# Performance work log

Hardware: AMD Instinct MI355X
Metric: run time of the kernel (lower is better)

The kernel has to match this reference:

```python
import jax, jax.numpy as jnp
import numpy as np

EPS = 1e-5  # BatchNorm1d default eps
NUM_HEADS = 8


def repbn(x, alpha, gamma, beta, rm, rv):
    # eval-mode RepBN over the channel (last) dim: BN(running stats) + alpha * x
    bn = (x - rm) * (gamma / jnp.sqrt(rv + EPS)) + beta
    return bn + alpha * x


def _forward(x, W_qkv, b_qkv, W_proj, b_proj, W1, b1, W2, b2, sa_w, sa_b,
             alpha1, gamma1, beta1, rm1, rv1, alpha2, gamma2, beta2, rm2, rv2):
    B, C, H, W = x.shape
    N = H * W
    D = C // NUM_HEADS
    t = x.reshape(B, C, N).transpose(0, 2, 1)  # [B, N, C]
    # --- FlashAttention (manual MHSA) ---
    qkv = (t @ W_qkv + b_qkv).reshape(B, N, 3, NUM_HEADS, D)
    q = qkv[:, :, 0].transpose(0, 2, 1, 3)  # [B, h, N, D]
    k = qkv[:, :, 1].transpose(0, 2, 1, 3)
    v = qkv[:, :, 2].transpose(0, 2, 1, 3)
    attn = jax.nn.softmax(jnp.einsum('bhnd,bhmd->bhnm', q, k) * (D ** -0.5), axis=-1)
    o = jnp.einsum('bhnm,bhmd->bhnd', attn, v).transpose(0, 2, 1, 3).reshape(B, N, C)
    o = o @ W_proj + b_proj
    # residual + blended norm (eval -> RepBN)
    t = repbn(t + o, alpha1, gamma1, beta1, rm1, rv1)
    # --- FFN with SpatialSILU activation ---
    h = t @ W1 + b1  # [B, N, cm]
    # depthwise 1x1 conv over the batch dim (channels==B per original unsqueeze(0))
    wgt = sa_w[:, None, None] * h + sa_b[:, None, None]
    h = h * jax.nn.sigmoid(wgt * h)
    f = h @ W2 + b2
    t = repbn(t + f, alpha2, gamma2, beta2, rm2, rv2)
    return t.transpose(0, 2, 1).reshape(B, C, H, W)


def setup_inputs() -> dict:
    key = jax.random.key(0)
    ks = jax.random.split(key, 8)
    B, C, H, W = 256, 256, 14, 14
    cm = 2048
    s = 0.02
    f32 = jnp.float32
    return {
        'x': jax.random.normal(ks[0], (B, C, H, W), f32),
        'W_qkv': jax.random.normal(ks[1], (C, 3 * C), f32) * s,
        'b_qkv': jnp.zeros((3 * C,), f32),
        'W_proj': jax.random.normal(ks[2], (C, C), f32) * s,
        'b_proj': jnp.zeros((C,), f32),
        'W1': jax.random.normal(ks[3], (C, cm), f32) * s,
        'b1': jnp.zeros((cm,), f32),
        'W2': jax.random.normal(ks[4], (cm, C), f32) * s,
        'b2': jnp.zeros((C,), f32),
        'sa_w': jax.random.normal(ks[5], (B,), f32) * s,
        'sa_b': jnp.zeros((B,), f32),
        'alpha1': jnp.ones((), f32),
        'gamma1': jnp.ones((C,), f32),
        'beta1': jnp.zeros((C,), f32),
        'rm1': jax.random.normal(ks[6], (C,), f32) * 0.1,
        'rv1': jnp.ones((C,), f32),
        'alpha2': jnp.ones((), f32),
        'gamma2': jnp.ones((C,), f32),
        'beta2': jnp.zeros((C,), f32),
        'rm2': jax.random.normal(ks[7], (C,), f32) * 0.1,
        'rv2': jnp.ones((C,), f32),
    }


def reference(x, W_qkv, b_qkv, W_proj, b_proj, W1, b1, W2, b2, sa_w, sa_b,
              alpha1, gamma1, beta1, rm1, rv1, alpha2, gamma2, beta2, rm2, rv2):
    return _forward(x, W_qkv, b_qkv, W_proj, b_proj, W1, b1, W2, b2, sa_w, sa_b,
                    alpha1, gamma1, beta1, rm1, rv1, alpha2, gamma2, beta2, rm2, rv2)
```

## Files before the change

kernel.cpp:

```cpp
#include <hip/hip_runtime.h>

using u16 = unsigned short;

typedef __bf16 bf16x8 __attribute__((ext_vector_type(8)));
typedef u16    u16x8  __attribute__((ext_vector_type(8)));
typedef float  f32x4  __attribute__((ext_vector_type(4)));

__device__ __forceinline__ float b2f(u16 u) {
    union { unsigned int i; float f; } c; c.i = ((unsigned int)u) << 16; return c.f;
}
__device__ __forceinline__ u16 f2b(float f) {
    union { float f; unsigned int i; } c; c.f = f;
    unsigned int i = c.i;
    return (u16)((i + 0x7FFFu + ((i >> 16) & 1u)) >> 16);
}

#define AS1 __attribute__((address_space(1)))
#define AS3 __attribute__((address_space(3)))
__device__ __forceinline__ void glds16(const u16* g, u16* l) {
    __builtin_amdgcn_global_load_lds((const AS1 void*)(const void*)g,
                                     (AS3 void*)(void*)l, 16, 0, 0);
}

__global__ void btrans_f2b(const float* __restrict__ in, u16* __restrict__ out, int R, int C) {
    __shared__ u16 tile[32][33];
    const int c0 = blockIdx.x * 32, r0 = blockIdx.y * 32;
    const size_t base = (size_t)blockIdx.z * R * C;
    const int tx = threadIdx.x, ty = threadIdx.y;
    #pragma unroll
    for (int i = ty; i < 32; i += 8) {
        int r = r0 + i, c = c0 + tx;
        tile[i][tx] = (r < R && c < C) ? f2b(in[base + (size_t)r * C + c]) : (u16)0;
    }
    __syncthreads();
    #pragma unroll
    for (int i = ty; i < 32; i += 8) {
        int c = c0 + i, r = r0 + tx;
        if (c < C && r < R) out[base + (size_t)c * R + r] = tile[tx][i];
    }
}

__global__ void btrans_b2f(const u16* __restrict__ in, float* __restrict__ out, int R, int C) {
    __shared__ u16 tile[32][33];
    const int c0 = blockIdx.x * 32, r0 = blockIdx.y * 32;
    const size_t base = (size_t)blockIdx.z * R * C;
    const int tx = threadIdx.x, ty = threadIdx.y;
    #pragma unroll
    for (int i = ty; i < 32; i += 8) {
        int r = r0 + i, c = c0 + tx;
        tile[i][tx] = (r < R && c < C) ? in[base + (size_t)r * C + c] : (u16)0;
    }
    __syncthreads();
    #pragma unroll
    for (int i = ty; i < 32; i += 8) {
        int c = c0 + i, r = r0 + tx;
        if (c < C && r < R) out[base + (size_t)c * R + r] = b2f(tile[tx][i]);
    }
}

template<int EPI>
__launch_bounds__(512, 4)
__global__ void gemm_bt(const u16* __restrict__ A, const u16* __restrict__ BT,
                        const float* __restrict__ bias, u16* __restrict__ C,
                        int M, int N, int K, int row0,
                        const u16* __restrict__ R0,
                        const float* __restrict__ g, const float* __restrict__ be,
                        const float* __restrict__ rmv, const float* __restrict__ rvv,
                        const float* __restrict__ alpha,
                        const float* __restrict__ saw, const float* __restrict__ sab) {
    __shared__ __align__(16) u16 ALds[2][128 * 32];
    __shared__ __align__(16) u16 BLds[2][128 * 32];
    const int tid  = threadIdx.x;
    const int wave = tid >> 6, lane = tid & 63;
    const int wm = wave >> 2, wn = wave & 3;
    const int quad = lane >> 4, l16 = lane & 15;

    const unsigned gx = gridDim.x;
    unsigned lin = blockIdx.y * gx + blockIdx.x;
    const unsigned nwg = gx * gridDim.y;
    const unsigned q8 = nwg >> 3, r8 = nwg & 7;
    const unsigned xcd = lin & 7, loc = lin >> 3;
    lin = (xcd < r8 ? xcd * (q8 + 1) : r8 * (q8 + 1) + (xcd - r8) * q8) + loc;
    const int m0 = (int)(lin / gx) * 128, n0 = (int)(lin % gx) * 128;

    const int srow = lane >> 2;
    const int scol = (((lane & 3) ^ ((srow >> 1) & 3)) * 8);
    const size_t aoff = (size_t)(m0 + wave * 16 + srow) * K + scol;
    const size_t boff = (size_t)(n0 + wave * 16 + srow) * K + scol;
    u16* aS = &ALds[0][0] + wave * 512;
    u16* bS = &BLds[0][0] + wave * 512;

    const int cfrag = (quad ^ ((l16 >> 1) & 3)) * 8;

    auto stage = [&](int buf, size_t kn) {
        const int bo = buf * 4096;
        glds16(A  + aoff + kn, aS + bo);
        glds16(BT + boff + kn, bS + bo);
    };

    f32x4 acc[4][2] = {};
    const int niter = K >> 5;

    stage(0, 0);

    for (int kt = 0; kt < niter; kt++) {
        const int cur = kt & 1, nxt = cur ^ 1;
        __syncthreads();
        if (kt + 1 < niter) stage(nxt, (size_t)(kt + 1) << 5);
        bf16x8 af[4], bfr[2];
        const u16* ab = &ALds[0][0] + cur * 4096;
        const u16* bb = &BLds[0][0] + cur * 4096;
        #pragma unroll
        for (int i = 0; i < 4; i++)
            af[i] = *(const bf16x8*)&ab[(wm * 64 + i * 16 + l16) * 32 + cfrag];
        #pragma unroll
        for (int j = 0; j < 2; j++)
            bfr[j] = *(const bf16x8*)&bb[(wn * 32 + j * 16 + l16) * 32 + cfrag];
        #pragma unroll
        for (int i = 0; i < 4; i++)
            #pragma unroll
            for (int j = 0; j < 2; j++)
                acc[i][j] = __builtin_amdgcn_mfma_f32_16x16x32_bf16(af[i], bfr[j], acc[i][j], 0, 0, 0);
    }

    float alphav = 0.f;
    if (EPI == 1) alphav = alpha[0];

    #pragma unroll
    for (int i = 0; i < 4; i++) {
        const int rowb = m0 + wm * 64 + i * 16 + quad * 4;
        #pragma unroll
        for (int r = 0; r < 4; r++) {
            const int row = rowb + r;
            float swv = 0.f, sbv = 0.f;
            if (EPI == 2) { int bidx = (row0 + row) / 196; swv = saw[bidx]; sbv = sab[bidx]; }
            #pragma unroll
            for (int j = 0; j < 2; j++) {
                const int col = n0 + wn * 32 + j * 16 + l16;
                float v = acc[i][j][r] + bias[col];
                const size_t off = (size_t)row * N + col;
                if (EPI == 0) {
                    C[off] = f2b(v);
                } else if (EPI == 1) {
                    float x  = v + b2f(R0[off]);
                    float sc = g[col] * rsqrtf(rvv[col] + 1e-5f);
                    float t  = (x - rmv[col]) * sc + be[col] + alphav * x;
                    C[off]  = f2b(t);
                } else {
                    float w   = swv * v + sbv;
                    float out = v / (1.f + __expf(-w * v));
                    C[off] = f2b(out);
                }
            }
        }
    }
}

__launch_bounds__(256)
__global__ void attn_kernel(const u16* __restrict__ qkv, u16* __restrict__ o) {
    __shared__ __align__(16) u16 Kb[224 * 32];
    __shared__ __align__(16) u16 Vt[32 * 232];
    __shared__ __align__(16) u16 Pl[4][16 * 232];
    const int tid  = threadIdx.x;
    const int wave = tid >> 6, lane = tid & 63;
    const int quad = lane >> 4, l16 = lane & 15;
    const int b = blockIdx.x >> 3, h = blockIdx.x & 7;
    const u16* qg = qkv + (size_t)b * 196 * 768 + h * 32;
    const float scale = 0.17677669529663687f;

    for (int idx = tid; idx < 896; idx += 256) {
        int row = idx >> 2, dp = (idx & 3) * 8;
        u16x8 kv = {};
        if (row < 196) kv = *(const u16x8*)&qg[(size_t)row * 768 + 256 + dp];
        *(u16x8*)&Kb[row * 32 + dp] = kv;
    }
    for (int idx = tid; idx < 224 * 32; idx += 256) {
        int row = idx >> 5, d = idx & 31;
        Vt[d * 232 + row] = (row < 196) ? qg[(size_t)row * 768 + 512 + d] : (u16)0;
    }
    for (int c = lane; c < 16 * 24; c += 64) {
        int m = c / 24, cc = 208 + (c % 24);
        Pl[wave][m * 232 + cc] = 0;
    }
    __syncthreads();

    for (int t = wave; t < 13; t += 4) {
        const int m0 = t * 16;
        bf16x8 aq = {};
        const int qrow = m0 + l16;
        if (qrow < 196) aq = *(const bf16x8*)&qg[(size_t)qrow * 768 + quad * 8];

        f32x4 s[13];
        #pragma unroll
        for (int ct = 0; ct < 13; ct++) {
            bf16x8 bk = *(const bf16x8*)&Kb[(ct * 16 + l16) * 32 + quad * 8];
            s[ct] = __builtin_amdgcn_mfma_f32_16x16x32_bf16(aq, bk, (f32x4){0.f, 0.f, 0.f, 0.f}, 0, 0, 0);
        }
        if (l16 >= 4) {
            #pragma unroll
            for (int r = 0; r < 4; r++) s[12][r] = -1e30f;
        }
        float mx[4] = {-1e30f, -1e30f, -1e30f, -1e30f};
        #pragma unroll
        for (int ct = 0; ct < 13; ct++)
            #pragma unroll
            for (int r = 0; r < 4; r++) mx[r] = fmaxf(mx[r], s[ct][r]);
        #pragma unroll
        for (int off = 1; off < 16; off <<= 1)
            #pragma unroll
            for (int r = 0; r < 4; r++) mx[r] = fmaxf(mx[r], __shfl_xor(mx[r], off, 64));
        float sum[4] = {0.f, 0.f, 0.f, 0.f};
        #pragma unroll
        for (int ct = 0; ct < 13; ct++) {
            #pragma unroll
            for (int r = 0; r < 4; r++) {
                float p = __expf((s[ct][r] - mx[r]) * scale);
                sum[r] += p;
                Pl[wave][(quad * 4 + r) * 232 + ct * 16 + l16] = f2b(p);
            }
        }
        #pragma unroll
        for (int off = 1; off < 16; off <<= 1)
            #pragma unroll
            for (int r = 0; r < 4; r++) sum[r] += __shfl_xor(sum[r], off, 64);
        float inv[4];
        #pragma unroll
        for (int r = 0; r < 4; r++) inv[r] = 1.f / sum[r];

        #pragma unroll
        for (int nt = 0; nt < 2; nt++) {
            f32x4 ao = {0.f, 0.f, 0.f, 0.f};
            #pragma unroll
            for (int kc = 0; kc < 7; kc++) {
                bf16x8 ap = *(const bf16x8*)&Pl[wave][l16 * 232 + kc * 32 + quad * 8];
                bf16x8 bv = *(const bf16x8*)&Vt[(nt * 16 + l16) * 232 + kc * 32 + quad * 8];
                ao = __builtin_amdgcn_mfma_f32_16x16x32_bf16(ap, bv, ao, 0, 0, 0);
            }
            #pragma unroll
            for (int r = 0; r < 4; r++) {
                const int gm = m0 + quad * 4 + r;
                if (gm < 196)
                    o[((size_t)b * 196 + gm) * 256 + h * 32 + nt * 16 + l16] = f2b(ao[r] * inv[r]);
            }
        }
    }
}

extern "C" void kernel_launch(void* const* d_in, const int* in_sizes, int n_in,
                              void* d_out, int out_size, void* d_ws, size_t ws_size,
                              hipStream_t stream) {
    const float* x      = (const float*)d_in[0];
    const float* Wqkv   = (const float*)d_in[1];
    const float* bqkv   = (const float*)d_in[2];
    const float* Wproj  = (const float*)d_in[3];
    const float* bproj  = (const float*)d_in[4];
    const float* W1     = (const float*)d_in[5];
    const float* b1     = (const float*)d_in[6];
    const float* W2     = (const float*)d_in[7];
    const float* b2     = (const float*)d_in[8];
    const float* saw    = (const float*)d_in[9];
    const float* sab    = (const float*)d_in[10];
    const float* alpha1 = (const float*)d_in[11];
    const float* g1     = (const float*)d_in[12];
    const float* be1    = (const float*)d_in[13];
    const float* rm1    = (const float*)d_in[14];
    const float* rv1    = (const float*)d_in[15];
    const float* alpha2 = (const float*)d_in[16];
    const float* g2     = (const float*)d_in[17];
    const float* be2    = (const float*)d_in[18];
    const float* rm2    = (const float*)d_in[19];
    const float* rv2    = (const float*)d_in[20];

    const int B = 256, Cc = 256, Np = 196, CM = 2048;
    const int M = B * Np;

    auto al = [](size_t s) { return (s + 255) & ~(size_t)255; };
    char* ws = (char*)d_ws;
    const size_t o_t0  = 0;
    const size_t o_t1  = o_t0 + al((size_t)M * Cc * 2);
    const size_t o_wq  = o_t1 + al((size_t)M * Cc * 2);
    const size_t o_wp  = o_wq + al((size_t)768 * Cc * 2);
    const size_t o_w1  = o_wp + al((size_t)Cc * Cc * 2);
    const size_t o_w2  = o_w1 + al((size_t)Cc * CM * 2);
    const size_t o_scr = o_w2 + al((size_t)CM * Cc * 2);
    const size_t S = (ws_size > o_scr) ? ws_size - o_scr : 0;

    u16* t0     = (u16*)(ws + o_t0);
    u16* t1b    = (u16*)(ws + o_t1);
    u16* WqkvT  = (u16*)(ws + o_wq);
    u16* WprojT = (u16*)(ws + o_wp);
    u16* W1T    = (u16*)(ws + o_w1);
    u16* W2T    = (u16*)(ws + o_w2);
    u16* scr    = (u16*)(ws + o_scr);
    u16* t2     = t0;
    u16* obuf   = (u16*)d_out;
    float* out  = (float*)d_out;

    int nq = 1; while (nq < 8 && ((size_t)(M / nq) * 768 * 2) > S) nq *= 2;
    const int nf_opts[7] = {1, 2, 4, 8, 14, 28, 56};
    int nf = 56;
    for (int i = 0; i < 7; ++i) {
        if (((size_t)(M / nf_opts[i]) * CM * 2) <= S) { nf = nf_opts[i]; break; }
    }
    const int Mq = M / nq, Bq = B / nq;
    const int Mf = M / nf;

    dim3 tb(32, 8, 1);
    btrans_f2b<<<dim3((Np + 31) / 32, (Cc + 31) / 32, B), tb, 0, stream>>>(x, t0, Cc, Np);
    btrans_f2b<<<dim3(768 / 32, Cc / 32, 1), tb, 0, stream>>>(Wqkv,  WqkvT,  Cc, 768);
    btrans_f2b<<<dim3(Cc  / 32, Cc / 32, 1), tb, 0, stream>>>(Wproj, WprojT, Cc, Cc);
    btrans_f2b<<<dim3(CM  / 32, Cc / 32, 1), tb, 0, stream>>>(W1,    W1T,    Cc, CM);
    btrans_f2b<<<dim3(Cc  / 32, CM / 32, 1), tb, 0, stream>>>(W2,    W2T,    CM, Cc);

    for (int c = 0; c < nq; ++c) {
        gemm_bt<0><<<dim3(768 / 128, Mq / 128), 512, 0, stream>>>(
            t0 + (size_t)c * Mq * Cc, WqkvT, bqkv, scr, Mq, 768, Cc, 0,
            nullptr, nullptr, nullptr, nullptr, nullptr, nullptr, nullptr, nullptr);
        attn_kernel<<<dim3(Bq * 8), 256, 0, stream>>>(scr, obuf + (size_t)c * Mq * Cc);
    }

    gemm_bt<1><<<dim3(Cc / 128, M / 128), 512, 0, stream>>>(
        obuf, WprojT, bproj, t1b, M, Cc, Cc, 0,
        t0, g1, be1, rm1, rv1, alpha1, nullptr, nullptr);

    for (int c = 0; c < nf; ++c) {
        gemm_bt<2><<<dim3(CM / 128, Mf / 128), 512, 0, stream>>>(
            t1b + (size_t)c * Mf * Cc, W1T, b1, scr, Mf, CM, Cc, c * Mf,
            nullptr, nullptr, nullptr, nullptr, nullptr, nullptr, saw, sab);
        gemm_bt<1><<<dim3(Cc / 128, Mf / 128), 512, 0, stream>>>(
            scr, W2T, b2, t2 + (size_t)c * Mf * Cc, Mf, Cc, CM, 0,
            t1b + (size_t)c * Mf * Cc, g2, be2, rm2, rv2, alpha2, nullptr, nullptr);
    }

    btrans_b2f<<<dim3((Cc + 31) / 32, (Np + 31) / 32, B), tb, 0, stream>>>(t2, out, Np, Cc);
}
```

Measured before the change: 572.4 us.

## Restructure GEMM epilogue with packed bf16 stores and LDS-staged residual

New measurement: 542.9 us. 5.2% less time.

```diff
diff --git a/kernel.cpp b/kernel.cpp
--- a/kernel.cpp
+++ b/kernel.cpp
@@ -13,6 +13,9 @@
     union { float f; unsigned int i; } c; c.f = f;
     unsigned int i = c.i;
     return (u16)((i + 0x7FFFu + ((i >> 16) & 1u)) >> 16);
+}
+__device__ __forceinline__ float u2f(unsigned int u) {
+    union { unsigned int i; float f; } c; c.i = u; return c.f;
 }
 
 #define AS1 __attribute__((address_space(1)))
@@ -68,8 +71,7 @@
                         const float* __restrict__ rmv, const float* __restrict__ rvv,
                         const float* __restrict__ alpha,
                         const float* __restrict__ saw, const float* __restrict__ sab) {
-    __shared__ __align__(16) u16 ALds[2][128 * 32];
-    __shared__ __align__(16) u16 BLds[2][128 * 32];
+    __shared__ __align__(16) u16 SL[16384];
     const int tid  = threadIdx.x;
     const int wave = tid >> 6, lane = tid & 63;
     const int wm = wave >> 2, wn = wave & 3;
@@ -87,10 +89,13 @@
     const int scol = (((lane & 3) ^ ((srow >> 1) & 3)) * 8);
     const size_t aoff = (size_t)(m0 + wave * 16 + srow) * K + scol;
     const size_t boff = (size_t)(n0 + wave * 16 + srow) * K + scol;
-    u16* aS = &ALds[0][0] + wave * 512;
-    u16* bS = &BLds[0][0] + wave * 512;
+    u16* aS = SL + wave * 512;
+    u16* bS = SL + 8192 + wave * 512;
 
     const int cfrag = (quad ^ ((l16 >> 1) & 3)) * 8;
+
+    f32x4 acc[4][2] = {};
+    const int niter = K >> 5;
 
     auto stage = [&](int buf, size_t kn) {
         const int bo = buf * 4096;
@@ -98,18 +103,12 @@
         glds16(BT + boff + kn, bS + bo);
     };
 
-    f32x4 acc[4][2] = {};
-    const int niter = K >> 5;
-
-    stage(0, 0);
-
-    for (int kt = 0; kt < niter; kt++) {
-        const int cur = kt & 1, nxt = cur ^ 1;
+    auto kstep = [&](int cur, int kt) {
         __syncthreads();
-        if (kt + 1 < niter) stage(nxt, (size_t)(kt + 1) << 5);
+        if (kt + 1 < niter) stage(cur ^ 1, (size_t)(kt + 1) << 5);
+        const u16* ab = SL + cur * 4096;
+        const u16* bb = SL + 8192 + cur * 4096;
         bf16x8 af[4], bfr[2];
-        const u16* ab = &ALds[0][0] + cur * 4096;
-        const u16* bb = &BLds[0][0] + cur * 4096;
         #pragma unroll
         for (int i = 0; i < 4; i++)
             af[i] = *(const bf16x8*)&ab[(wm * 64 + i * 16 + l16) * 32 + cfrag];
@@ -121,37 +120,83 @@
             #pragma unroll
             for (int j = 0; j < 2; j++)
                 acc[i][j] = __builtin_amdgcn_mfma_f32_16x16x32_bf16(af[i], bfr[j], acc[i][j], 0, 0, 0);
-    }
+    };
+
+    stage(0, 0);
+    int kt = 0;
+    for (; kt + 2 <= niter; kt += 2) { kstep(0, kt); kstep(1, kt + 1); }
+    if (kt < niter) kstep(kt & 1, kt);
+
+    __syncthreads();
 
     float alphav = 0.f;
     if (EPI == 1) alphav = alpha[0];
 
+    if (EPI == 1) {
+        #pragma unroll
+        for (int c = tid; c < 2048; c += 512) {
+            int row = c >> 4, colc = (c & 15) * 8;
+            *(u16x8*)&SL[row * 128 + colc] =
+                *(const u16x8*)&R0[(size_t)(m0 + row) * N + n0 + colc];
+        }
+        __syncthreads();
+    }
+
+    float biasv[2], k0v[2], k1v[2];
+    #pragma unroll
+    for (int j = 0; j < 2; j++) {
+        const int col = n0 + wn * 32 + j * 16 + l16;
+        biasv[j] = bias[col];
+        if (EPI == 1) {
+            float sc = g[col] * rsqrtf(rvv[col] + 1e-5f);
+            k1v[j] = sc + alphav;
+            k0v[j] = be[col] - rmv[col] * sc;
+        }
+    }
+
+    const int dup = l16 & 1;
+    const int pr  = l16 >> 1;
+    u16* Crow = C + (size_t)(m0 + wm * 64 + quad * 4 + 2 * dup) * N
+                  + (n0 + wn * 32 + pr * 2);
+
     #pragma unroll
     for (int i = 0; i < 4; i++) {
-        const int rowb = m0 + wm * 64 + i * 16 + quad * 4;
-        #pragma unroll
-        for (int r = 0; r < 4; r++) {
-            const int row = rowb + r;
-            float swv = 0.f, sbv = 0.f;
-            if (EPI == 2) { int bidx = (row0 + row) / 196; swv = saw[bidx]; sbv = sab[bidx]; }
-            #pragma unroll
-            for (int j = 0; j < 2; j++) {
-                const int col = n0 + wn * 32 + j * 16 + l16;
-                float v = acc[i][j][r] + bias[col];
-                const size_t off = (size_t)row * N + col;
-                if (EPI == 0) {
-                    C[off] = f2b(v);
-                } else if (EPI == 1) {
-                    float x  = v + b2f(R0[off]);
-                    float sc = g[col] * rsqrtf(rvv[col] + 1e-5f);
-                    float t  = (x - rmv[col]) * sc + be[col] + alphav * x;
-                    C[off]  = f2b(t);
-                } else {
-                    float w   = swv * v + sbv;
-                    float out = v / (1.f + __expf(-w * v));
-                    C[off] = f2b(out);
+        #pragma unroll
+        for (int j = 0; j < 2; j++) {
+            float vv[4];
+            #pragma unroll
+            for (int r = 0; r < 4; r++) {
+                float v = acc[i][j][r] + biasv[j];
+                if (EPI == 1) {
+                    const int rowL = wm * 64 + i * 16 + quad * 4 + r;
+                    const int colp = wn * 32 + j * 16 + (l16 & ~1);
+                    unsigned rd = *(const unsigned*)&SL[rowL * 128 + colp];
+                    unsigned fb = dup ? (rd & 0xffff0000u) : (rd << 16);
+                    float x = v + u2f(fb);
+                    v = fmaf(x, k1v[j], k0v[j]);
+                } else if (EPI == 2) {
+                    const int row = row0 + m0 + wm * 64 + i * 16 + quad * 4 + r;
+                    const int bidx = row / 196;
+                    float w = fmaf(saw[bidx], v, sab[bidx]);
+                    v = v / (1.f + __expf(-w * v));
                 }
-            }
+                vv[r] = v;
+            }
+            unsigned D[4];
+            #pragma unroll
+            for (int r = 0; r < 4; r++) {
+                float o  = __shfl_xor(vv[r], 1, 64);
+                float lo = dup ? o : vv[r];
+                float hi = dup ? vv[r] : o;
+                unsigned d;
+                asm("v_cvt_pk_bf16_f32 %0, %1, %2" : "=v"(d) : "v"(lo), "v"(hi));
+                D[r] = d;
+            }
+            unsigned s0 = dup ? D[2] : D[0];
+            unsigned s1 = dup ? D[3] : D[1];
+            u16* p = Crow + (size_t)i * 16 * N + j * 16;
+            *(unsigned*)p       = s0;
+            *(unsigned*)(p + N) = s1;
         }
     }
 }
```
